# Optimization experiments

Measured on AMD Instinct MI355X. Metric: run time of the kernel, lower is better.

Reference implementation:

```python
import jax, jax.numpy as jnp
import numpy as np

D_MODEL = 1024
N_EXPERTS = 8
TOP_K = 2
CAP_FACTOR = 1.0
HIDDEN = 2816  # multiple_of*ceil(int(2*4*d/3)/multiple_of) with multiple_of=256


def setup_inputs() -> dict:
    key = jax.random.key(0)
    ks = jax.random.split(key, 8)
    B, S = 2, 2048
    s = 0.02
    return {
        "x": jax.random.normal(ks[0], (B, S, D_MODEL), jnp.float32),
        "noise": jax.random.normal(ks[1], (B, S, N_EXPERTS), jnp.float32),
        "router_w": jax.random.normal(ks[2], (N_EXPERTS, D_MODEL), jnp.float32) * s,
        "router_b": jnp.zeros((N_EXPERTS,), jnp.float32),
        "noise_w": jax.random.normal(ks[3], (N_EXPERTS, D_MODEL), jnp.float32) * s,
        "noise_b": jnp.zeros((N_EXPERTS,), jnp.float32),
        "w1": jax.random.normal(ks[4], (N_EXPERTS, HIDDEN, D_MODEL), jnp.float32) * s,
        "w3": jax.random.normal(ks[5], (N_EXPERTS, HIDDEN, D_MODEL), jnp.float32) * s,
        "w2": jax.random.normal(ks[6], (N_EXPERTS, D_MODEL, HIDDEN), jnp.float32) * s,
    }


def reference(x, noise, router_w, router_b, noise_w, noise_b, w1, w3, w2):
    B, S, d = x.shape
    N = B * S
    capacity = int(N * TOP_K / N_EXPERTS * CAP_FACTOR)
    flat_x = x.reshape(N, d)

    # noisy top-k router
    logits = flat_x @ router_w.T + router_b                      # [N, E]
    noise_logits = flat_x @ noise_w.T + noise_b                  # [N, E]
    noisy = logits + noise.reshape(N, N_EXPERTS) * jax.nn.softplus(noise_logits)
    topv, topi = jax.lax.top_k(noisy, TOP_K)                     # [N, k]
    # softmax over sparse (-inf filled) logits == softmax over top-k values
    gw = jax.nn.softmax(topv, axis=-1)                           # [N, k]

    updates = jnp.zeros_like(flat_x)
    tok_ids = jnp.arange(N, dtype=jnp.int32)
    for e in range(N_EXPERTS):
        hit = topi == e                                          # [N, k]
        gate = jnp.sum(gw * hit, axis=-1)                        # [N]
        m = jnp.any(hit, axis=-1)                                # token routed to e
        pos = jnp.cumsum(m.astype(jnp.int32)) - 1                # rank in flat order
        keep = m & (pos < capacity)                              # capacity truncation (first-come)
        slot = jnp.where(keep, pos, capacity)                    # dropped tokens -> overflow slot
        # gather tokens into fixed-capacity buffer (slot `capacity` is a trash slot)
        buf = jnp.zeros((capacity + 1, d), x.dtype).at[slot].set(flat_x)
        tok = jnp.full((capacity + 1,), N, jnp.int32).at[slot].set(tok_ids)
        xb = buf[:capacity]
        # SwiGLU FFN: w2( silu(x w1^T) * (x w3^T) )
        h = jax.nn.silu(xb @ w1[e].T) * (xb @ w3[e].T)           # [cap, H]
        o = h @ w2[e].T                                          # [cap, d]
        tke = tok[:capacity]
        g = jnp.where(tke < N, gate[jnp.clip(tke, 0, N - 1)], 0.0)
        # scatter-combine; index N drops (empty slots)
        updates = updates.at[tke].add(o * g[:, None], mode="drop")
    return updates.reshape(B, S, d)
```

## Files before the change

kernel.cpp:

```cpp
#include <hip/hip_runtime.h>


#define D_MODEL 1024
#define HIDDEN 2816
#define N_TOK 4096
#define CAP 1024

typedef __attribute__((ext_vector_type(8))) short short8;
typedef __attribute__((ext_vector_type(4))) float f32x4;

__device__ __forceinline__ unsigned short f2bf(float f) {
  unsigned int u = __float_as_uint(f);
  u += 0x7fffu + ((u >> 16) & 1u);
  return (unsigned short)(u >> 16);
}
__device__ __forceinline__ float bf2f(unsigned short h) {
  return __uint_as_float(((unsigned int)h) << 16);
}
__device__ __forceinline__ unsigned cvtpk(float lo, float hi) {
  unsigned r;
  asm("v_cvt_pk_bf16_f32 %0, %1, %2" : "=v"(r) : "v"(lo), "v"(hi));
  return r;
}

template <int Ncnt> __device__ __forceinline__ void waitv() {
  if constexpr (Ncnt == 12)     asm volatile("s_waitcnt vmcnt(12)" ::: "memory");
  else if constexpr (Ncnt == 4) asm volatile("s_waitcnt vmcnt(4)" ::: "memory");
  else                          asm volatile("s_waitcnt vmcnt(0)" ::: "memory");
}

__global__ void router_kernel(const float* __restrict__ x, const float* __restrict__ noise,
                              const float* __restrict__ rw, const float* __restrict__ rb,
                              const float* __restrict__ nw, const float* __restrict__ nb,
                              int* __restrict__ topi, float* __restrict__ gall,
                              int* __restrict__ slot) {
  int wid = threadIdx.x >> 6;
  int lane = threadIdx.x & 63;
  int t = blockIdx.x * 4 + wid;
  if (t >= N_TOK) return;
  const float* xr = x + (size_t)t * D_MODEL;
  double accL[8] = {0,0,0,0,0,0,0,0};
  double accN[8] = {0,0,0,0,0,0,0,0};
  for (int i = 0; i < 4; ++i) {
    int kb = (i * 64 + lane) * 4;
    float4 xv = *(const float4*)(xr + kb);
#pragma unroll
    for (int e = 0; e < 8; ++e) {
      float4 wv = *(const float4*)(rw + e * D_MODEL + kb);
      accL[e] += (double)xv.x * wv.x + (double)xv.y * wv.y + (double)xv.z * wv.z + (double)xv.w * wv.w;
      float4 nv = *(const float4*)(nw + e * D_MODEL + kb);
      accN[e] += (double)xv.x * nv.x + (double)xv.y * nv.y + (double)xv.z * nv.z + (double)xv.w * nv.w;
    }
  }
#pragma unroll
  for (int e = 0; e < 8; ++e) {
    for (int s = 32; s > 0; s >>= 1) {
      accL[e] += __shfl_xor(accL[e], s);
      accN[e] += __shfl_xor(accN[e], s);
    }
  }
  if (lane == 0) {
    double noisy[8];
#pragma unroll
    for (int e = 0; e < 8; ++e) {
      double lg = accL[e] + (double)rb[e];
      double nl = accN[e] + (double)nb[e];
      double sp = (nl > 0.0 ? nl : 0.0) + log1p(exp(-fabs(nl)));
      noisy[e] = lg + (double)noise[t * 8 + e] * sp;
    }
    int i0 = 0;
    for (int e = 1; e < 8; ++e) if (noisy[e] > noisy[i0]) i0 = e;
    int i1 = -1;
    for (int e = 0; e < 8; ++e) { if (e == i0) continue; if (i1 < 0 || noisy[e] > noisy[i1]) i1 = e; }
    double g0 = 1.0 / (1.0 + exp(noisy[i1] - noisy[i0]));
    topi[t * 2] = i0; topi[t * 2 + 1] = i1;
    gall[t * 2] = (float)g0; gall[t * 2 + 1] = (float)(1.0 - g0);
    slot[t * 2] = -1; slot[t * 2 + 1] = -1;
  }
}

__global__ void scan_kernel(const int* __restrict__ topi,
                            int* __restrict__ slot, int* __restrict__ tok_list) {
  int e = blockIdx.x;
  int tid = threadIdx.x;
  int lane = tid & 63, wid = tid >> 6;
  __shared__ int wsum[16];
  __shared__ int base_s;
  tok_list[e * CAP + tid] = -1;
  if (tid == 0) base_s = 0;
  __syncthreads();
  for (int chunk = 0; chunk < N_TOK / 1024; ++chunk) {
    int t = chunk * 1024 + tid;
    int i0 = topi[t * 2], i1 = topi[t * 2 + 1];
    bool m = (i0 == e) || (i1 == e);
    unsigned long long mask = __ballot(m);
    int excl = __popcll(mask & ((1ull << lane) - 1ull));
    if (lane == 0) wsum[wid] = __popcll(mask);
    __syncthreads();
    int base = base_s;
    int woff = 0;
    for (int w = 0; w < wid; ++w) woff += wsum[w];
    int pos = base + woff + excl;
    if (m && pos < CAP) {
      tok_list[e * CAP + pos] = t;
      if (i0 == e) slot[t * 2] = pos; else slot[t * 2 + 1] = pos;
    }
    __syncthreads();
    if (tid == 0) {
      int s = 0;
      for (int w = 0; w < 16; ++w) s += wsum[w];
      base_s = base + s;
    }
    __syncthreads();
  }
}

__global__ void gather_kernel(const float* __restrict__ x, const int* __restrict__ tok_list,
                              unsigned short* __restrict__ xb) {
  int row = blockIdx.x;
  int tok = tok_list[row];
  unsigned short* dst = xb + (size_t)row * D_MODEL + threadIdx.x * 4;
  if (tok < 0) {
    *(ushort4*)dst = make_ushort4(0, 0, 0, 0);
  } else {
    float4 v = *(const float4*)(x + (size_t)tok * D_MODEL + threadIdx.x * 4);
    *(ushort4*)dst = make_ushort4(f2bf(v.x), f2bf(v.y), f2bf(v.z), f2bf(v.w));
  }
}

template <int NOUT, int K, int MODE>
__global__ __launch_bounds__(512, 1)
void gemm_moe(const unsigned short* __restrict__ Ab, const float* __restrict__ W0,
              const float* __restrict__ W1, void* __restrict__ OUT) {
  constexpr int ABYTES = 32768;
  constexpr int BUFSZ = ABYTES + 32768;
  constexpr int KT = K / 64;
  constexpr int SK = (MODE == 2) ? 2 : 1;
  constexpr int KTS = KT / SK;
  constexpr int BNCOL = (MODE == 2) ? 256 : 128;
  constexpr int NBN = NOUT / BNCOL;
  constexpr int NWG = 8 * 4 * NBN * SK;

  __shared__ char smem[2 * BUFSZ];

  int lid = blockIdx.x;
  int swz = (lid & 7) * (NWG / 8) + (lid >> 3);
  constexpr int PERE = 4 * NBN * SK;
  int e = swz / PERE;
  int r = swz - e * PERE;
  int bm = r / (NBN * SK);
  int r2 = r - bm * (NBN * SK);
  int bn = r2 / SK;
  int sk = r2 - bn * SK;
  int kt0 = sk * KTS;

  const unsigned short* A = Ab + (size_t)e * CAP * K;
  int tid = threadIdx.x, lane = tid & 63, wid = tid >> 6;
  int wr = wid >> 2, wc = wid & 3;
  int lane15 = lane & 15, lhi = lane >> 4, l7 = lane & 7;

  int lrow = lane >> 3;
  int lcol = ((lane & 7) ^ lrow) * 8;
  const unsigned short* Abase = A + (size_t)(bm * 256 + lrow) * K + lcol;

  auto ASTAGE = [&](int ktile, int buf) {
    char* lb = smem + buf * BUFSZ;
#pragma unroll
    for (int i = 0; i < 4; ++i) {
      int c = wid * 4 + i;
      const unsigned short* g = Abase + (size_t)(c * 8) * K + ktile * 64;
      __builtin_amdgcn_global_load_lds((const __attribute__((address_space(1))) void*)g,
                                       (__attribute__((address_space(3))) void*)(lb + c * 1024), 16, 0, 0);
    }
  };

  const float* wptr[4];
  int woff[4];
#pragma unroll
  for (int i = 0; i < 4; ++i) {
    int L = i * 512 + tid;
    int p = (L >> 3) & 127;
    int ks = L & 7;
    const float* Wb = (i >> 1) ? W1 : W0;
    wptr[i] = Wb + (size_t)e * NOUT * K + (size_t)(bn * BNCOL + p) * K + ks * 8;
    woff[i] = ABYTES + (i >> 1) * 16384 + p * 128 + ((ks ^ (p & 7)) * 16);
  }

  float4 rbuf[4][2];
  auto BLOAD = [&](int ktile) {
#pragma unroll
    for (int i = 0; i < 4; ++i) {
      const float* s = wptr[i] + (size_t)ktile * 64;
      rbuf[i][0] = *(const float4*)(s);
      rbuf[i][1] = *(const float4*)(s + 4);
    }
  };
  auto BWRITE = [&](char* lb) {
#pragma unroll
    for (int i = 0; i < 4; ++i) {
      uint4 v;
      v.x = cvtpk(rbuf[i][0].x, rbuf[i][0].y);
      v.y = cvtpk(rbuf[i][0].z, rbuf[i][0].w);
      v.z = cvtpk(rbuf[i][1].x, rbuf[i][1].y);
      v.w = cvtpk(rbuf[i][1].z, rbuf[i][1].w);
      *(uint4*)(lb + woff[i]) = v;
    }
  };

  int sw0 = ((0 + lhi) ^ l7) * 16;
  int sw1 = ((4 + lhi) ^ l7) * 16;

  f32x4 acc[8][2][2] = {};

  BLOAD(kt0);
  __builtin_amdgcn_sched_barrier(0);
  ASTAGE(kt0, 0);
  __builtin_amdgcn_sched_barrier(0);
  waitv<4>();
  BWRITE(smem);
  BLOAD(kt0 + 1);
  __builtin_amdgcn_sched_barrier(0);
  ASTAGE(kt0 + 1, 1);
  waitv<12>();
  asm volatile("s_waitcnt lgkmcnt(0)" ::: "memory");
  __builtin_amdgcn_sched_barrier(0);
  __builtin_amdgcn_s_barrier();
  __builtin_amdgcn_sched_barrier(0);

  for (int ktl = 0; ktl < KTS; ++ktl) {
    char* cb = smem + (ktl & 1) * BUFSZ;
    char* nbuf = smem + ((ktl + 1) & 1) * BUFSZ;
    if (ktl + 1 < KTS) {
      waitv<4>();
      BWRITE(nbuf);
      if (ktl + 2 < KTS) {
        BLOAD(kt0 + ktl + 2);
        __builtin_amdgcn_sched_barrier(0);
      }
    }
    short8 a0[8], b0[2][2], a1[8], b1[2][2];
#pragma unroll
    for (int w = 0; w < 2; ++w)
#pragma unroll
      for (int n = 0; n < 2; ++n)
        b0[w][n] = *(const short8*)(cb + ABYTES + w * 16384 + wc * 4096 + n * 2048 + lane15 * 128 + sw0);
#pragma unroll
    for (int m = 0; m < 8; ++m)
      a0[m] = *(const short8*)(cb + wr * 16384 + m * 2048 + lane15 * 128 + sw0);
    __builtin_amdgcn_s_setprio(1);
#pragma unroll
    for (int m = 0; m < 8; ++m)
#pragma unroll
      for (int w = 0; w < 2; ++w)
#pragma unroll
        for (int n = 0; n < 2; ++n)
          acc[m][w][n] = __builtin_amdgcn_mfma_f32_16x16x32_bf16(a0[m], b0[w][n], acc[m][w][n], 0, 0, 0);
    __builtin_amdgcn_s_setprio(0);
#pragma unroll
    for (int w = 0; w < 2; ++w)
#pragma unroll
      for (int n = 0; n < 2; ++n)
        b1[w][n] = *(const short8*)(cb + ABYTES + w * 16384 + wc * 4096 + n * 2048 + lane15 * 128 + sw1);
#pragma unroll
    for (int m = 0; m < 8; ++m)
      a1[m] = *(const short8*)(cb + wr * 16384 + m * 2048 + lane15 * 128 + sw1);
    __builtin_amdgcn_sched_barrier(0);
    __builtin_amdgcn_s_barrier();
    __builtin_amdgcn_sched_barrier(0);
    if (ktl + 2 < KTS) ASTAGE(kt0 + ktl + 2, ktl & 1);
    __builtin_amdgcn_s_setprio(1);
#pragma unroll
    for (int m = 0; m < 8; ++m)
#pragma unroll
      for (int w = 0; w < 2; ++w)
#pragma unroll
        for (int n = 0; n < 2; ++n)
          acc[m][w][n] = __builtin_amdgcn_mfma_f32_16x16x32_bf16(a1[m], b1[w][n], acc[m][w][n], 0, 0, 0);
    __builtin_amdgcn_s_setprio(0);
    if (ktl + 1 < KTS) {
      if (ktl + 2 < KTS) waitv<12>();
      else               waitv<0>();
      asm volatile("s_waitcnt lgkmcnt(0)" ::: "memory");
      __builtin_amdgcn_sched_barrier(0);
      __builtin_amdgcn_s_barrier();
      __builtin_amdgcn_sched_barrier(0);
    }
  }

  if constexpr (MODE == 1) {
    unsigned short* H = (unsigned short*)OUT + (size_t)e * CAP * NOUT;
#pragma unroll
    for (int m = 0; m < 8; ++m) {
#pragma unroll
      for (int n = 0; n < 2; ++n) {
        int row0 = bm * 256 + wr * 128 + m * 16 + lhi * 4;
        int col = bn * 128 + wc * 32 + n * 16 + lane15;
#pragma unroll
        for (int j = 0; j < 4; ++j) {
          float g1 = acc[m][0][n][j];
          float g3 = acc[m][1][n][j];
          float hv = g1 / (1.0f + __expf(-g1)) * g3;
          H[(size_t)(row0 + j) * NOUT + col] = f2bf(hv);
        }
      }
    }
  } else {
    float* P = (float*)OUT + (size_t)sk * 8 * CAP * NOUT + (size_t)e * CAP * NOUT;
#pragma unroll
    for (int m = 0; m < 8; ++m) {
#pragma unroll
      for (int w = 0; w < 2; ++w) {
#pragma unroll
        for (int n = 0; n < 2; ++n) {
          int row0 = bm * 256 + wr * 128 + m * 16 + lhi * 4;
          int col = bn * BNCOL + w * 128 + wc * 32 + n * 16 + lane15;
#pragma unroll
          for (int j = 0; j < 4; ++j)
            P[(size_t)(row0 + j) * NOUT + col] = acc[m][w][n][j];
        }
      }
    }
  }
}

__global__ void combine_kernel(const float* __restrict__ ob, const int* __restrict__ topi,
                               const float* __restrict__ gall, const int* __restrict__ slot,
                               float* __restrict__ out) {
  int t = blockIdx.x;
  int d = threadIdx.x * 4;
  const size_t HALF = (size_t)8 * CAP * D_MODEL;
  float4 r = make_float4(0.f, 0.f, 0.f, 0.f);
#pragma unroll
  for (int k = 0; k < 2; ++k) {
    int s = slot[t * 2 + k];
    if (s >= 0) {
      int e = topi[t * 2 + k];
      float g = gall[t * 2 + k];
      size_t base = ((size_t)e * CAP + s) * D_MODEL + d;
      float4 a = *(const float4*)(ob + base);
      float4 b = *(const float4*)(ob + HALF + base);
      r.x += g * (a.x + b.x); r.y += g * (a.y + b.y);
      r.z += g * (a.z + b.z); r.w += g * (a.w + b.w);
    }
  }
  *(float4*)(out + (size_t)t * D_MODEL + d) = r;
}

extern "C" void kernel_launch(void* const* d_in, const int* in_sizes, int n_in,
                              void* d_out, int out_size, void* d_ws, size_t ws_size,
                              hipStream_t stream) {
  const float* x     = (const float*)d_in[0];
  const float* noise = (const float*)d_in[1];
  const float* rw    = (const float*)d_in[2];
  const float* rb    = (const float*)d_in[3];
  const float* nw    = (const float*)d_in[4];
  const float* nb    = (const float*)d_in[5];
  const float* w1    = (const float*)d_in[6];
  const float* w3    = (const float*)d_in[7];
  const float* w2    = (const float*)d_in[8];
  float* out = (float*)d_out;

  char* ws = (char*)d_ws;
  size_t off = 0;
  auto alloc = [&](size_t bytes) -> void* {
    void* p = ws + off;
    off += (bytes + 255) & ~(size_t)255;
    return p;
  };
  unsigned short* xb = (unsigned short*)alloc((size_t)8 * CAP * D_MODEL * 2);
  unsigned short* h  = (unsigned short*)alloc((size_t)8 * CAP * HIDDEN * 2);
  float*          ob = (float*)alloc((size_t)2 * 8 * CAP * D_MODEL * 4);
  int*   topi  = (int*)alloc(N_TOK * 2 * 4);
  float* gall  = (float*)alloc(N_TOK * 2 * 4);
  int*   slot  = (int*)alloc(N_TOK * 2 * 4);
  int*   tokl  = (int*)alloc(8 * CAP * 4);
  (void)ws_size; (void)in_sizes; (void)n_in; (void)out_size;

  router_kernel<<<N_TOK / 4, 256, 0, stream>>>(x, noise, rw, rb, nw, nb, topi, gall, slot);
  scan_kernel<<<8, 1024, 0, stream>>>(topi, slot, tokl);
  gather_kernel<<<8 * CAP, 256, 0, stream>>>(x, tokl, xb);

  gemm_moe<HIDDEN, D_MODEL, 1><<<dim3(704), 512, 0, stream>>>(xb, w1, w3, (void*)h);

  gemm_moe<D_MODEL, HIDDEN, 2><<<dim3(256), 512, 0, stream>>>(
      h, w2, w2 + (size_t)128 * HIDDEN, (void*)ob);

  combine_kernel<<<N_TOK, 256, 0, stream>>>(ob, topi, gall, slot, out);
}
```

Baseline: 308.1 us.

## Deepen weight register prefetch to two tiles ahead with ping-pong buffers

The fp32 weight (B) loads now use two register buffers that alternate, so global loads for tile k+3 are issued while tile k+1 is converted and written to LDS. This removes the vmcnt wait that sat before each BWRITE and gives weight loads a full extra iteration of latency hiding. The loop is unrolled by two so the buffer choice is static, and the vmcnt thresholds are adjusted to match. In exchange it holds another 32 VGPRs of prefetch data, which may lower occupancy or cause spills, and the loop assumes KTS is even.

After: 803.5 us. +160.8%, slower.

```diff
diff --git a/kernel.cpp b/kernel.cpp
--- a/kernel.cpp
+++ b/kernel.cpp
@@ -24,9 +24,11 @@
 }
 
 template <int Ncnt> __device__ __forceinline__ void waitv() {
-  if constexpr (Ncnt == 12)     asm volatile("s_waitcnt vmcnt(12)" ::: "memory");
-  else if constexpr (Ncnt == 4) asm volatile("s_waitcnt vmcnt(4)" ::: "memory");
-  else                          asm volatile("s_waitcnt vmcnt(0)" ::: "memory");
+  if constexpr (Ncnt == 16)      asm volatile("s_waitcnt vmcnt(16)" ::: "memory");
+  else if constexpr (Ncnt == 12) asm volatile("s_waitcnt vmcnt(12)" ::: "memory");
+  else if constexpr (Ncnt == 8)  asm volatile("s_waitcnt vmcnt(8)" ::: "memory");
+  else if constexpr (Ncnt == 4)  asm volatile("s_waitcnt vmcnt(4)" ::: "memory");
+  else                           asm volatile("s_waitcnt vmcnt(0)" ::: "memory");
 }
 
 __global__ void router_kernel(const float* __restrict__ x, const float* __restrict__ noise,
@@ -164,13 +166,12 @@
   const unsigned short* Abase = A + (size_t)(bm * 256 + lrow) * K + lcol;
 
   auto ASTAGE = [&](int ktile, int buf) {
-    char* lb = smem + buf * BUFSZ;
 #pragma unroll
     for (int i = 0; i < 4; ++i) {
       int c = wid * 4 + i;
       const unsigned short* g = Abase + (size_t)(c * 8) * K + ktile * 64;
       __builtin_amdgcn_global_load_lds((const __attribute__((address_space(1))) void*)g,
-                                       (__attribute__((address_space(3))) void*)(lb + c * 1024), 16, 0, 0);
+                                       (__attribute__((address_space(3))) void*)(smem + buf * BUFSZ + c * 1024), 16, 0, 0);
     }
   };
 
@@ -186,23 +187,23 @@
     woff[i] = ABYTES + (i >> 1) * 16384 + p * 128 + ((ks ^ (p & 7)) * 16);
   }
 
-  float4 rbuf[4][2];
-  auto BLOAD = [&](int ktile) {
+  float4 rbA[4][2], rbB[4][2];
+  auto BLOAD = [&](int ktile, float4 (&rb)[4][2]) {
 #pragma unroll
     for (int i = 0; i < 4; ++i) {
       const float* s = wptr[i] + (size_t)ktile * 64;
-      rbuf[i][0] = *(const float4*)(s);
-      rbuf[i][1] = *(const float4*)(s + 4);
-    }
-  };
-  auto BWRITE = [&](char* lb) {
+      rb[i][0] = *(const float4*)(s);
+      rb[i][1] = *(const float4*)(s + 4);
+    }
+  };
+  auto BWRITE = [&](char* lb, const float4 (&rb)[4][2]) {
 #pragma unroll
     for (int i = 0; i < 4; ++i) {
       uint4 v;
-      v.x = cvtpk(rbuf[i][0].x, rbuf[i][0].y);
-      v.y = cvtpk(rbuf[i][0].z, rbuf[i][0].w);
-      v.z = cvtpk(rbuf[i][1].x, rbuf[i][1].y);
-      v.w = cvtpk(rbuf[i][1].z, rbuf[i][1].w);
+      v.x = cvtpk(rb[i][0].x, rb[i][0].y);
+      v.y = cvtpk(rb[i][0].z, rb[i][0].w);
+      v.z = cvtpk(rb[i][1].x, rb[i][1].y);
+      v.w = cvtpk(rb[i][1].z, rb[i][1].w);
       *(uint4*)(lb + woff[i]) = v;
     }
   };
@@ -212,32 +213,28 @@
 
   f32x4 acc[8][2][2] = {};
 
-  BLOAD(kt0);
+  BLOAD(kt0, rbA);
+  BLOAD(kt0 + 1, rbB);
   __builtin_amdgcn_sched_barrier(0);
   ASTAGE(kt0, 0);
-  __builtin_amdgcn_sched_barrier(0);
-  waitv<4>();
-  BWRITE(smem);
-  BLOAD(kt0 + 1);
-  __builtin_amdgcn_sched_barrier(0);
   ASTAGE(kt0 + 1, 1);
+  __builtin_amdgcn_sched_barrier(0);
+  waitv<16>();
+  BWRITE(smem, rbA);
+  BLOAD(kt0 + 2, rbA);
+  __builtin_amdgcn_sched_barrier(0);
   waitv<12>();
   asm volatile("s_waitcnt lgkmcnt(0)" ::: "memory");
   __builtin_amdgcn_sched_barrier(0);
   __builtin_amdgcn_s_barrier();
   __builtin_amdgcn_sched_barrier(0);
 
-  for (int ktl = 0; ktl < KTS; ++ktl) {
+  auto ITER = [&](int ktl, float4 (&rbW)[4][2]) {
     char* cb = smem + (ktl & 1) * BUFSZ;
     char* nbuf = smem + ((ktl + 1) & 1) * BUFSZ;
-    if (ktl + 1 < KTS) {
-      waitv<4>();
-      BWRITE(nbuf);
-      if (ktl + 2 < KTS) {
-        BLOAD(kt0 + ktl + 2);
-        __builtin_amdgcn_sched_barrier(0);
-      }
-    }
+    if (ktl + 1 < KTS) BWRITE(nbuf, rbW);
+    if (ktl + 3 < KTS) BLOAD(kt0 + ktl + 3, rbW);
+    __builtin_amdgcn_sched_barrier(0);
     short8 a0[8], b0[2][2], a1[8], b1[2][2];
 #pragma unroll
     for (int w = 0; w < 2; ++w)
@@ -278,13 +275,20 @@
           acc[m][w][n] = __builtin_amdgcn_mfma_f32_16x16x32_bf16(a1[m], b1[w][n], acc[m][w][n], 0, 0, 0);
     __builtin_amdgcn_s_setprio(0);
     if (ktl + 1 < KTS) {
-      if (ktl + 2 < KTS) waitv<12>();
-      else               waitv<0>();
+      if (ktl + 3 < KTS)      waitv<12>();
+      else if (ktl + 2 < KTS) waitv<4>();
+      else                    waitv<0>();
       asm volatile("s_waitcnt lgkmcnt(0)" ::: "memory");
       __builtin_amdgcn_sched_barrier(0);
       __builtin_amdgcn_s_barrier();
       __builtin_amdgcn_sched_barrier(0);
     }
+  };
+
+#pragma unroll 1
+  for (int kt2 = 0; kt2 < KTS; kt2 += 2) {
+    ITER(kt2, rbB);
+    ITER(kt2 + 1, rbA);
   }
 
   if constexpr (MODE == 1) {
```
